# Performance work log

Measured on AMD Instinct MI355X. Metric: run time of the kernel, lower is better.

Reference implementation:

```python
import math
import jax, jax.numpy as jnp
from jax import lax
import numpy as np

B, C, M, N = 8, 512, 64, 64
DN = ('NCHW', 'OIHW', 'NCHW')


def dct_mat(n):
    # Orthonormal DCT-II basis, matching the torch construction.
    i = jnp.arange(n, dtype=jnp.float32)
    A = jnp.cos(jnp.outer(i, i + 0.5) * (math.pi / n)) * np.float32(math.sqrt(2.0 / n))
    return A.at[0].divide(np.float32(math.sqrt(2.0)))


def setup_inputs() -> dict:
    key = jax.random.key(0)
    ks = jax.random.split(key, 7)
    s = 0.05
    x = jax.random.normal(ks[0], (B, C, M, N), dtype=jnp.float32)
    # 4 conv branches, each: 1x1 512->128, 3x3 dil=2 128->128, 1x1 128->128
    W1 = jax.random.normal(ks[1], (4, 128, 512, 1, 1), dtype=jnp.float32) * s
    b1 = jax.random.normal(ks[2], (4, 128), dtype=jnp.float32) * s
    W2 = jax.random.normal(ks[3], (4, 128, 128, 3, 3), dtype=jnp.float32) * s
    b2 = jax.random.normal(ks[4], (4, 128), dtype=jnp.float32) * s
    W3 = jax.random.normal(ks[5], (4, 128, 128, 1, 1), dtype=jnp.float32) * s
    b3 = jax.random.normal(ks[6], (4, 128), dtype=jnp.float32) * s
    return {"x": x, "W1": W1, "b1": b1, "W2": W2, "b2": b2, "W3": W3, "b3": b3}


def dct3d_topk(x):
    b, c, m, n = x.shape
    Ac, Ar, Ak = dct_mat(n), dct_mat(m), dct_mat(c)
    # separable 3D DCT: along N, then M, then C
    t = jnp.einsum('kn,bcmn->bcmk', Ac, x)
    t = jnp.einsum('km,bcmn->bckn', Ar, t)
    D = jnp.einsum('kc,bcmn->bkmn', Ak, t)
    total = b * c * m * n
    absD = jnp.abs(D)
    s = jnp.sort(absD.reshape(-1))  # ascending; kth-largest = s[total-k]
    recons = []
    for k in (total // 4, total // 16, total // 64, total // 256):
        thr = s[total - k]
        Dm = jnp.where(absD >= thr, D, jnp.float32(0))
        y = jnp.einsum('kc,bkmn->bcmn', Ak, Dm)   # inverse along C
        y = jnp.einsum('km,bckn->bcmn', Ar, y)    # inverse along M
        y = jnp.einsum('kn,bcmk->bcmn', Ac, y)    # inverse along N
        recons.append(y)
    return jnp.stack(recons)  # [4, B, C, M, N]


def conv_branch(h, w1, c1, w2, c2, w3, c3):
    h = lax.conv_general_dilated(h, w1, (1, 1), 'VALID', dimension_numbers=DN)
    h = jax.nn.relu(h + c1[None, :, None, None])
    h = lax.conv_general_dilated(h, w2, (1, 1), ((2, 2), (2, 2)), rhs_dilation=(2, 2), dimension_numbers=DN)
    h = jax.nn.relu(h + c2[None, :, None, None])
    h = lax.conv_general_dilated(h, w3, (1, 1), 'VALID', dimension_numbers=DN)
    return jax.nn.relu(h + c3[None, :, None, None])


def reference(x, W1, b1, W2, b2, W3, b3):
    d = dct3d_topk(x)
    outs = [conv_branch(d[i], W1[i], b1[i], W2[i], b2[i], W3[i], b3[i]) for i in range(4)]
    w = jax.nn.softmax(jnp.concatenate(outs, axis=1), axis=1)
    return x * w + x
```

## Files before the change

### kernel.cpp

```cpp
#include <hip/hip_runtime.h>
#include <math.h>

#define NB   8
#define NC   512
#define SP   4096
#define TOT  16777216L
static const double PI_D = 3.14159265358979323846;

typedef short s16x8 __attribute__((ext_vector_type(8)));
typedef float f32x4 __attribute__((ext_vector_type(4)));
typedef unsigned short u16;

#define OFF_T    0L
#define OFF_CAND 0L
#define OFF_CNT  8388608L
#define OFF_P2   8392704L
#define OFF_P3   9441280L
#define OFF_H2R  9965568L
#define OFF_H3R  9969664L
#define OFF_H1P  0L
#define OFF_X2   8388608L
#define OFF_THI  16777216L
#define OFF_H1   16777216L
#define OFF_D    25165824L
#define OFF_H2   25165824L
#define OFF_AK   41943040L
#define OFF_AKH  42205184L
#define OFF_AKL  42336256L
#define OFF_ACT  42467328L
#define OFF_GBF  42468352L
#define OFF_W2A  42599424L
#define OFF_W3B  42894336L
#define OFF_HIST 42927104L
#define OFF_SEL  42937344L
#define OFF_THR  42937360L
#define OFF_AC   42937368L

__device__ inline u16 bfr(float x) {
    unsigned u = __float_as_uint(x);
    unsigned r = u + 0x7fffu + ((u >> 16) & 1u);
    return (u16)(r >> 16);
}
__device__ inline float bff(u16 h) { return __uint_as_float(((unsigned)h) << 16); }

#define MFMA(a, b, c) __builtin_amdgcn_mfma_f32_16x16x32_bf16((a), (b), (c), 0, 0, 0)

__global__ void k_ctab(float* __restrict__ ctab) {
    int m = blockIdx.x * 256 + threadIdx.x;
    if (m < 2048) ctab[m] = (float)cos(PI_D * (double)m / 1024.0);
}

__global__ void k_build_mats(const float* __restrict__ ctab,
                             u16* __restrict__ Akh, u16* __restrict__ Akl,
                             u16* __restrict__ AcT, float* __restrict__ Ac) {
    int idx = blockIdx.x * 256 + threadIdx.x;
    if (idx < 512 * 512) {
        int i = idx >> 9, j = idx & 511;
        float c = ctab[(i * (2 * j + 1)) & 2047];
        float f = c * (i == 0 ? 0.04419417382415922f : 0.0625f);
        u16 h = bfr(f);
        Akh[idx] = h;
        Akl[idx] = bfr(f - bff(h));
    }
    if (idx < 64 * 64) {
        int i = idx >> 6, j = idx & 63;
        float c = ctab[(8 * i * (2 * j + 1)) & 2047];
        Ac[idx] = c * (i == 0 ? 0.125f : 0.17677669529663687f);
        int n = idx >> 6, np = idx & 63;
        float w = ctab[(8 * np * (2 * n + 1)) & 2047];
        AcT[idx] = bfr(w * (np == 0 ? 0.125f : 0.17677669529663687f));
    }
}

__global__ void k_zero(unsigned* __restrict__ p, int n) {
    int i = blockIdx.x * 256 + threadIdx.x;
    if (i < n) p[i] = 0u;
}

__global__ __launch_bounds__(256, 2) void k_gmm(const float* __restrict__ W1,
                                                const u16* __restrict__ Akh, const u16* __restrict__ Akl,
                                                u16* __restrict__ G) {
    __shared__ __align__(16) short Wh[128 * 40];
    __shared__ __align__(16) short Wl[128 * 40];
    __shared__ __align__(16) short Qh[128 * 40];
    __shared__ __align__(16) short Ql[128 * 40];
    const int p0 = blockIdx.y * 128, kc0 = blockIdx.x * 128;
    const int tid = threadIdx.x;
    const int lane = tid & 63, wave = tid >> 6;
    const int fr = lane & 15, qd = lane >> 4;
    const int mq = (wave >> 1) * 64, nq = (wave & 1) * 64;
    f32x4 acc[4][4];
#pragma unroll
    for (int i = 0; i < 4; ++i)
#pragma unroll
        for (int j = 0; j < 4; ++j) acc[i][j] = (f32x4){0.f, 0.f, 0.f, 0.f};
    const float* Pg = W1 + (long)p0 * 512;
    const u16* Qgh = Akh + (long)kc0 * 512;
    const u16* Qgl = Akl + (long)kc0 * 512;
    const int r0 = tid >> 2, q40 = (tid & 3) * 8;
    float4 pa4[2], pb4[2];
    s16x8 qsh[2], qsl[2];
#pragma unroll
    for (int j = 0; j < 2; ++j) {
        int r = r0 + j * 64;
        const float* src = &Pg[(long)r * 512 + q40];
        pa4[j] = *(const float4*)src;
        pb4[j] = *(const float4*)(src + 4);
        qsh[j] = *(const s16x8*)&Qgh[(long)r * 512 + q40];
        qsl[j] = *(const s16x8*)&Qgl[(long)r * 512 + q40];
    }
    for (int ch = 0; ch < 16; ++ch) {
        __syncthreads();
#pragma unroll
        for (int j = 0; j < 2; ++j) {
            int r = r0 + j * 64;
            float f[8] = {pa4[j].x, pa4[j].y, pa4[j].z, pa4[j].w,
                          pb4[j].x, pb4[j].y, pb4[j].z, pb4[j].w};
            s16x8 vh, vl;
#pragma unroll
            for (int q = 0; q < 8; ++q) {
                u16 h = bfr(f[q]);
                vh[q] = (short)h;
                vl[q] = (short)bfr(f[q] - bff(h));
            }
            *(s16x8*)&Wh[r * 40 + q40] = vh;
            *(s16x8*)&Wl[r * 40 + q40] = vl;
            *(s16x8*)&Qh[r * 40 + q40] = qsh[j];
            *(s16x8*)&Ql[r * 40 + q40] = qsl[j];
        }
        __syncthreads();
        if (ch < 15) {
            const int kn = (ch + 1) * 32;
#pragma unroll
            for (int j = 0; j < 2; ++j) {
                int r = r0 + j * 64;
                const float* src = &Pg[(long)r * 512 + kn + q40];
                pa4[j] = *(const float4*)src;
                pb4[j] = *(const float4*)(src + 4);
                qsh[j] = *(const s16x8*)&Qgh[(long)r * 512 + kn + q40];
                qsl[j] = *(const s16x8*)&Qgl[(long)r * 512 + kn + q40];
            }
        }
        s16x8 qfh[4], qfl[4];
#pragma unroll
        for (int j = 0; j < 4; ++j) {
            qfh[j] = *(const s16x8*)&Qh[(nq + 16 * j + fr) * 40 + qd * 8];
            qfl[j] = *(const s16x8*)&Ql[(nq + 16 * j + fr) * 40 + qd * 8];
        }
#pragma unroll
        for (int i = 0; i < 4; ++i) {
            s16x8 wh = *(const s16x8*)&Wh[(mq + 16 * i + fr) * 40 + qd * 8];
            s16x8 wl = *(const s16x8*)&Wl[(mq + 16 * i + fr) * 40 + qd * 8];
#pragma unroll
            for (int j = 0; j < 4; ++j) {
                acc[i][j] = MFMA(wh, qfh[j], acc[i][j]);
                acc[i][j] = MFMA(wh, qfl[j], acc[i][j]);
                acc[i][j] = MFMA(wl, qfh[j], acc[i][j]);
            }
        }
    }
#pragma unroll
    for (int i = 0; i < 4; ++i)
#pragma unroll
        for (int j = 0; j < 4; ++j) {
            int rowb = mq + 16 * i + qd * 4;
            int col = kc0 + nq + 16 * j + fr;
#pragma unroll
            for (int r = 0; r < 4; ++r)
                G[(long)(p0 + rowb + r) * 512 + col] = bfr(acc[i][j][r]);
        }
}

__global__ void k_wprep(const float* __restrict__ W2, const float* __restrict__ W3,
                        u16* __restrict__ W2a, u16* __restrict__ W3b) {
    int idx = blockIdx.x * 256 + threadIdx.x;
    if (idx < 4 * 128 * 1152) {
        int k = idx % 1152;
        int oi = idx / 1152;
        int t = k >> 7, ci = k & 127;
        W2a[idx] = bfr(W2[((long)oi * 128 + ci) * 9 + t]);
    }
    if (idx < 65536) W3b[idx] = bfr(W3[idx]);
}

__global__ __launch_bounds__(256, 3) void k_tile_fwd(const float* __restrict__ in,
                                                     u16* __restrict__ out16,
                                                     const float* __restrict__ A64) {
    __shared__ __align__(16) float Ms[64][68];
    __shared__ __align__(16) float Ts[64][68];
    __shared__ __align__(16) float Ss[64][68];
    const int tid = threadIdx.x;
    const long tile = blockIdx.x;
    const float* __restrict__ src = in + tile * 4096;
    u16* __restrict__ dst = out16 + tile * 4096;
    for (int idx = tid; idx < 4096; idx += 256) {
        int r = idx >> 6, c = idx & 63;
        Ms[c][r] = A64[idx];
        Ts[r][c] = src[idx];
    }
    __syncthreads();
    const int tx = tid & 15, ty = tid >> 4;
    float acc[4][4];
#pragma unroll
    for (int i = 0; i < 4; ++i)
#pragma unroll
        for (int j = 0; j < 4; ++j) acc[i][j] = 0.f;
#pragma unroll 4
    for (int j = 0; j < 64; ++j) {
        float4 bv = *(const float4*)&Ms[j][tx * 4];
        float a0 = Ts[ty * 4 + 0][j], a1 = Ts[ty * 4 + 1][j];
        float a2 = Ts[ty * 4 + 2][j], a3 = Ts[ty * 4 + 3][j];
        acc[0][0] += a0 * bv.x; acc[0][1] += a0 * bv.y; acc[0][2] += a0 * bv.z; acc[0][3] += a0 * bv.w;
        acc[1][0] += a1 * bv.x; acc[1][1] += a1 * bv.y; acc[1][2] += a1 * bv.z; acc[1][3] += a1 * bv.w;
        acc[2][0] += a2 * bv.x; acc[2][1] += a2 * bv.y; acc[2][2] += a2 * bv.z; acc[2][3] += a2 * bv.w;
        acc[3][0] += a3 * bv.x; acc[3][1] += a3 * bv.y; acc[3][2] += a3 * bv.z; acc[3][3] += a3 * bv.w;
    }
#pragma unroll
    for (int i = 0; i < 4; ++i)
        *(float4*)&Ss[ty * 4 + i][tx * 4] = make_float4(acc[i][0], acc[i][1], acc[i][2], acc[i][3]);
    __syncthreads();
#pragma unroll
    for (int i = 0; i < 4; ++i)
#pragma unroll
        for (int j = 0; j < 4; ++j) acc[i][j] = 0.f;
#pragma unroll 4
    for (int j = 0; j < 64; ++j) {
        float4 av = *(const float4*)&Ms[j][ty * 4];
        float4 sv = *(const float4*)&Ss[j][tx * 4];
        acc[0][0] += av.x * sv.x; acc[0][1] += av.x * sv.y; acc[0][2] += av.x * sv.z; acc[0][3] += av.x * sv.w;
        acc[1][0] += av.y * sv.x; acc[1][1] += av.y * sv.y; acc[1][2] += av.y * sv.z; acc[1][3] += av.y * sv.w;
        acc[2][0] += av.z * sv.x; acc[2][1] += av.z * sv.y; acc[2][2] += av.z * sv.z; acc[2][3] += av.z * sv.w;
        acc[3][0] += av.w * sv.x; acc[3][1] += av.w * sv.y; acc[3][2] += av.w * sv.z; acc[3][3] += av.w * sv.w;
    }
#pragma unroll
    for (int i = 0; i < 4; ++i) {
        ushort4 pk;
        pk.x = bfr(acc[i][0]); pk.y = bfr(acc[i][1]);
        pk.z = bfr(acc[i][2]); pk.w = bfr(acc[i][3]);
        *(ushort4*)&dst[(ty * 4 + i) * 64 + tx * 4] = pk;
    }
}

__global__ __launch_bounds__(256) void k_tsplit(const u16* __restrict__ t16,
                                                u16* __restrict__ thi) {
    __shared__ float Ls[64][65];
    const int b = blockIdx.z, cg = blockIdx.y, pg = blockIdx.x;
    const int tid = threadIdx.x;
    const u16* src = t16 + ((long)b * 512 + cg * 64) * 4096 + pg * 64;
#pragma unroll
    for (int j = 0; j < 2; ++j) {
        int idx = tid + j * 256;
        int c = idx >> 3, p8 = (idx & 7) * 8;
        s16x8 v = *(const s16x8*)&src[(long)c * 4096 + p8];
#pragma unroll
        for (int q = 0; q < 8; ++q) Ls[c][p8 + q] = bff((u16)v[q]);
    }
    __syncthreads();
#pragma unroll
    for (int j = 0; j < 2; ++j) {
        int idx = tid + j * 256;
        int p = idx >> 3, c8 = idx & 7;
        s16x8 vh;
#pragma unroll
        for (int q = 0; q < 8; ++q) vh[q] = (short)bfr(Ls[c8 * 8 + q][p]);
        long addr = ((long)b * 4096 + pg * 64 + p) * 512 + cg * 64 + c8 * 8;
        *(s16x8*)&thi[addr] = vh;
    }
}

__global__ __launch_bounds__(256, 4) void k_cgemm(const u16* __restrict__ thi,
                                                  const u16* __restrict__ Akh, const u16* __restrict__ Akl,
                                                  float* __restrict__ D, unsigned* __restrict__ g1) {
    __shared__ __align__(16) short Ph[128 * 40];
    __shared__ __align__(16) short Qh[128 * 40];
    __shared__ __align__(16) short Ql[128 * 40];
    __shared__ unsigned hh[2048];
    const int b = blockIdx.z;
    const int p0 = blockIdx.y * 128, kc0 = blockIdx.x * 128;
    const int tid = threadIdx.x;
    const int lane = tid & 63, wave = tid >> 6;
    const int fr = lane & 15, qd = lane >> 4;
    const int mq = (wave >> 1) * 64, nq = (wave & 1) * 64;
    for (int t = tid; t < 2048; t += 256) hh[t] = 0u;
    f32x4 acc[4][4];
#pragma unroll
    for (int i = 0; i < 4; ++i)
#pragma unroll
        for (int j = 0; j < 4; ++j) acc[i][j] = (f32x4){0.f, 0.f, 0.f, 0.f};
    const u16* Pgh = thi + ((long)b * 4096 + p0) * 512;
    const u16* Qgh = Akh + (long)kc0 * 512;
    const u16* Qgl = Akl + (long)kc0 * 512;
    const int r0 = tid >> 2, q40 = (tid & 3) * 8;
    s16x8 psh[2], qsh[2], qsl[2];
#pragma unroll
    for (int j = 0; j < 2; ++j) {
        int r = r0 + j * 64;
        psh[j] = *(const s16x8*)&Pgh[(long)r * 512 + q40];
        qsh[j] = *(const s16x8*)&Qgh[(long)r * 512 + q40];
        qsl[j] = *(const s16x8*)&Qgl[(long)r * 512 + q40];
    }
    for (int ch = 0; ch < 16; ++ch) {
        __syncthreads();
#pragma unroll
        for (int j = 0; j < 2; ++j) {
            int r = r0 + j * 64;
            *(s16x8*)&Ph[r * 40 + q40] = psh[j];
            *(s16x8*)&Qh[r * 40 + q40] = qsh[j];
            *(s16x8*)&Ql[r * 40 + q40] = qsl[j];
        }
        __syncthreads();
        if (ch < 15) {
            const int kn = (ch + 1) * 32;
#pragma unroll
            for (int j = 0; j < 2; ++j) {
                int r = r0 + j * 64;
                psh[j] = *(const s16x8*)&Pgh[(long)r * 512 + kn + q40];
                qsh[j] = *(const s16x8*)&Qgh[(long)r * 512 + kn + q40];
                qsl[j] = *(const s16x8*)&Qgl[(long)r * 512 + kn + q40];
            }
        }
        s16x8 qfh[4], qfl[4];
#pragma unroll
        for (int j = 0; j < 4; ++j) {
            qfh[j] = *(const s16x8*)&Qh[(nq + 16 * j + fr) * 40 + qd * 8];
            qfl[j] = *(const s16x8*)&Ql[(nq + 16 * j + fr) * 40 + qd * 8];
        }
#pragma unroll
        for (int i = 0; i < 4; ++i) {
            s16x8 ph = *(const s16x8*)&Ph[(mq + 16 * i + fr) * 40 + qd * 8];
#pragma unroll
            for (int j = 0; j < 4; ++j) {
                acc[i][j] = MFMA(ph, qfh[j], acc[i][j]);
                acc[i][j] = MFMA(ph, qfl[j], acc[i][j]);
            }
        }
    }
#pragma unroll
    for (int i = 0; i < 4; ++i)
#pragma unroll
        for (int j = 0; j < 4; ++j) {
            int rowb = mq + 16 * i + qd * 4;
            int col = kc0 + nq + 16 * j + fr;
#pragma unroll
            for (int r = 0; r < 4; ++r) {
                float v = acc[i][j][r];
                D[((long)b * 4096 + p0 + rowb + r) * 512 + col] = v;
                unsigned bin = __float_as_uint(fabsf(v)) >> 19;
                atomicAdd(&hh[bin & 2047u], 1u << ((bin >> 11) << 4));
            }
        }
    __syncthreads();
    for (int t = tid; t < 2048; t += 256) {
        unsigned c = hh[t];
        unsigned lo = c & 0xffffu, hi = c >> 16;
        if (lo) atomicAdd(&g1[t], lo);
        if (hi) atomicAdd(&g1[t + 2048], hi);
    }
}

__global__ void k_scan1(const unsigned* __restrict__ hist, unsigned* __restrict__ sel) {
    __shared__ unsigned chunk[256];
    __shared__ unsigned above[256];
    const int t = threadIdx.x;
    unsigned s = 0;
#pragma unroll
    for (int j = 0; j < 16; ++j) s += hist[t * 16 + j];
    chunk[t] = s;
    __syncthreads();
    if (t == 0) {
        unsigned a = 0;
        for (int c = 255; c >= 0; --c) { above[c] = a; a += chunk[c]; }
    }
    __syncthreads();
    const unsigned kv[4] = {4194304u, 1048576u, 262144u, 65536u};
    unsigned run = above[t];
    for (int j = 15; j >= 0; --j) {
        unsigned bin = t * 16 + j;
        unsigned hb = hist[bin];
        unsigned Sab = run;
        run += hb;
#pragma unroll
        for (int i = 0; i < 4; ++i)
            if (run >= kv[i] && Sab < kv[i]) { sel[i] = bin; sel[4 + i] = kv[i] - Sab; }
    }
}

__global__ __launch_bounds__(256) void k_compact(const float4* __restrict__ D,
                                                 const unsigned* __restrict__ sel,
                                                 unsigned* __restrict__ cand,
                                                 unsigned* __restrict__ cnt) {
    __shared__ unsigned lctr;
    if (threadIdx.x == 0) lctr = 0u;
    __syncthreads();
    const unsigned p0 = sel[0], p1 = sel[1], p2 = sel[2], p3 = sel[3];
    const int lane = threadIdx.x & 63;
    unsigned* slice = cand + (long)blockIdx.x * 4096;
    const long n4 = TOT / 4;
    for (long idx = (long)blockIdx.x * 256 + threadIdx.x; idx < n4; idx += (long)gridDim.x * 256) {
        float4 v = D[idx];
        float f[4] = {v.x, v.y, v.z, v.w};
#pragma unroll
        for (int q = 0; q < 4; ++q) {
            unsigned u = __float_as_uint(fabsf(f[q]));
            unsigned pre = u >> 19;
            bool m = (pre == p0) | (pre == p1) | (pre == p2) | (pre == p3);
            unsigned long long mask = __ballot(m);
            if (mask) {
                int leader = __ffsll((long long)mask) - 1;
                unsigned base = 0;
                if (lane == leader) base = atomicAdd(&lctr, (unsigned)__popcll(mask));
                base = (unsigned)__shfl((int)base, leader);
                if (m) {
                    unsigned pos = base + (unsigned)__popcll(mask & ((1ULL << lane) - 1ULL));
                    if (pos < 4096u) slice[pos] = u;
                }
            }
        }
    }
    __syncthreads();
    if (threadIdx.x == 0) cnt[blockIdx.x] = lctr < 4096u ? lctr : 4096u;
}

__global__ __launch_bounds__(256) void k_hist2c(const unsigned* __restrict__ cand,
                                                const unsigned* __restrict__ cnt,
                                                const unsigned* __restrict__ sel,
                                                unsigned* __restrict__ partial) {
    __shared__ unsigned h[4096];
    for (int i = threadIdx.x; i < 4096; i += 256) h[i] = 0u;
    __syncthreads();
    const unsigned p0 = sel[0], p1 = sel[1], p2 = sel[2], p3 = sel[3];
    for (int s = 0; s < 8; ++s) {
        int slice = blockIdx.x * 8 + s;
        unsigned n = cnt[slice];
        const unsigned* L = cand + (long)slice * 4096;
        for (unsigned i = threadIdx.x; i < n; i += 256) {
            unsigned u = L[i];
            unsigned pre = u >> 19, mid = (u >> 9) & 1023u;
            if (pre == p0) atomicAdd(&h[mid], 1u);
            else if (pre == p1) atomicAdd(&h[1024 + mid], 1u);
            else if (pre == p2) atomicAdd(&h[2048 + mid], 1u);
            else if (pre == p3) atomicAdd(&h[3072 + mid], 1u);
        }
    }
    __syncthreads();
    unsigned* dst = partial + (long)blockIdx.x * 4096;
    for (int i = threadIdx.x; i < 4096; i += 256) dst[i] = h[i];
}

__global__ __launch_bounds__(256) void k_red(const unsigned* __restrict__ partial,
                                             unsigned* __restrict__ out, int nbins, int nrows) {
    int bin = blockIdx.x * 256 + threadIdx.x;
    if (bin >= nbins) return;
    unsigned s = 0;
#pragma unroll 16
    for (int r = 0; r < nrows; ++r) s += partial[(long)r * nbins + bin];
    out[bin] = s;
}

__global__ void k_scan2(const unsigned* __restrict__ hist2, unsigned* __restrict__ sel) {
    __shared__ unsigned chunk[256];
    __shared__ unsigned above[256];
    const int t = threadIdx.x;
    for (int i = 0; i < 4; ++i) {
        const unsigned* h = hist2 + i * 1024;
        unsigned r = sel[4 + i];
        unsigned s = h[t * 4] + h[t * 4 + 1] + h[t * 4 + 2] + h[t * 4 + 3];
        chunk[t] = s;
        __syncthreads();
        if (t == 0) {
            unsigned a = 0;
            for (int c = 255; c >= 0; --c) { above[c] = a; a += chunk[c]; }
        }
        __syncthreads();
        unsigned run = above[t];
        for (int j = 3; j >= 0; --j) {
            unsigned bin = t * 4 + j;
            unsigned hb = h[bin];
            unsigned Sab = run;
            run += hb;
            if (run >= r && Sab < r) { sel[8 + i] = bin; sel[12 + i] = r - Sab; }
        }
        __syncthreads();
    }
}

__global__ __launch_bounds__(256) void k_hist3c(const unsigned* __restrict__ cand,
                                                const unsigned* __restrict__ cnt,
                                                const unsigned* __restrict__ sel,
                                                unsigned* __restrict__ partial) {
    __shared__ unsigned h[2048];
    for (int i = threadIdx.x; i < 2048; i += 256) h[i] = 0u;
    __syncthreads();
    unsigned pre2[4];
#pragma unroll
    for (int i = 0; i < 4; ++i) pre2[i] = (sel[i] << 10) | sel[8 + i];
    for (int s = 0; s < 8; ++s) {
        int slice = blockIdx.x * 8 + s;
        unsigned n = cnt[slice];
        const unsigned* L = cand + (long)slice * 4096;
        for (unsigned i = threadIdx.x; i < n; i += 256) {
            unsigned u = L[i];
            unsigned p = u >> 9, low = u & 511u;
            if (p == pre2[0]) atomicAdd(&h[low], 1u);
            else if (p == pre2[1]) atomicAdd(&h[512 + low], 1u);
            else if (p == pre2[2]) atomicAdd(&h[1024 + low], 1u);
            else if (p == pre2[3]) atomicAdd(&h[1536 + low], 1u);
        }
    }
    __syncthreads();
    unsigned* dst = partial + (long)blockIdx.x * 2048;
    for (int i = threadIdx.x; i < 2048; i += 256) dst[i] = h[i];
}

__global__ void k_scan3(const unsigned* __restrict__ hist3, const unsigned* __restrict__ sel,
                        float* __restrict__ thr) {
    __shared__ unsigned chunk[256];
    __shared__ unsigned above[256];
    const int t = threadIdx.x;
    for (int i = 0; i < 4; ++i) {
        const unsigned* h = hist3 + i * 512;
        unsigned r = sel[12 + i];
        unsigned s = h[t * 2] + h[t * 2 + 1];
        chunk[t] = s;
        __syncthreads();
        if (t == 0) {
            unsigned a = 0;
            for (int c = 255; c >= 0; --c) { above[c] = a; a += chunk[c]; }
        }
        __syncthreads();
        unsigned run = above[t];
        for (int j = 1; j >= 0; --j) {
            unsigned bin = t * 2 + j;
            unsigned hb = h[bin];
            unsigned Sab = run;
            run += hb;
            if (run >= r && Sab < r)
                thr[i] = __uint_as_float((sel[i] << 19) | (sel[8 + i] << 9) | bin);
        }
        __syncthreads();
    }
}

__global__ __launch_bounds__(256, 4) void k_conv1(const float* __restrict__ D, const u16* __restrict__ Gb,
                                                  const float* __restrict__ thrp, u16* __restrict__ h1pre) {
    __shared__ __align__(16) short Pt[128 * 40];
    __shared__ __align__(16) short Qt[128 * 40];
    const int b = blockIdx.z, br = blockIdx.y, p0 = blockIdx.x * 128;
    const int z2 = br * 8 + b;
    const float thr = thrp[br];
    const int tid = threadIdx.x;
    const int lane = tid & 63, wave = tid >> 6;
    const int fr = lane & 15, qd = lane >> 4;
    const int mq = (wave >> 1) * 64, nq = (wave & 1) * 64;
    f32x4 acc[4][4];
#pragma unroll
    for (int i = 0; i < 4; ++i)
#pragma unroll
        for (int j = 0; j < 4; ++j) acc[i][j] = (f32x4){0.f, 0.f, 0.f, 0.f};
    const float* Pg = D + ((long)b * 4096 + p0) * 512;
    const u16* Qg = Gb + (long)br * 65536;
    const int r0 = tid >> 2, q40 = (tid & 3) * 8;
    float4 da[2], db[2];
#pragma unroll
    for (int j = 0; j < 2; ++j) {
        const float* src = &Pg[(long)(r0 + j * 64) * 512 + q40];
        da[j] = *(const float4*)src;
        db[j] = *(const float4*)(src + 4);
    }
    for (int ch = 0; ch < 16; ++ch) {
        const int k0 = ch * 32;
        __syncthreads();
#pragma unroll
        for (int j = 0; j < 2; ++j) {
            int r = r0 + j * 64;
            s16x8 m;
            float f[8] = {da[j].x, da[j].y, da[j].z, da[j].w, db[j].x, db[j].y, db[j].z, db[j].w};
#pragma unroll
            for (int q = 0; q < 8; ++q) m[q] = (short)(fabsf(f[q]) >= thr ? bfr(f[q]) : (u16)0);
            *(s16x8*)&Pt[r * 40 + q40] = m;
            *(s16x8*)&Qt[r * 40 + q40] = *(const s16x8*)&Qg[(long)r * 512 + k0 + q40];
        }
        __syncthreads();
        if (ch < 15) {
            const int kn = k0 + 32;
#pragma unroll
            for (int j = 0; j < 2; ++j) {
                const float* src = &Pg[(long)(r0 + j * 64) * 512 + kn + q40];
                da[j] = *(const float4*)src;
                db[j] = *(const float4*)(src + 4);
            }
        }
        s16x8 qb[4];
#pragma unroll
        for (int j = 0; j < 4; ++j) qb[j] = *(const s16x8*)&Qt[(nq + 16 * j + fr) * 40 + qd * 8];
#pragma unroll
        for (int i = 0; i < 4; ++i) {
            s16x8 pa = *(const s16x8*)&Pt[(mq + 16 * i + fr) * 40 + qd * 8];
#pragma unroll
            for (int j = 0; j < 4; ++j) acc[i][j] = MFMA(pa, qb[j], acc[i][j]);
        }
    }
#pragma unroll
    for (int i = 0; i < 4; ++i)
#pragma unroll
        for (int j = 0; j < 4; ++j) {
            int rowb = p0 + mq + 16 * i + qd * 4;
            int o = nq + 16 * j + fr;
            ushort4 pk;
            pk.x = bfr(acc[i][j][0]); pk.y = bfr(acc[i][j][1]);
            pk.z = bfr(acc[i][j][2]); pk.w = bfr(acc[i][j][3]);
            *(ushort4*)&h1pre[((long)z2 * 128 + o) * 4096 + rowb] = pk;
        }
}

__global__ __launch_bounds__(256, 4) void k_idct1(const u16* __restrict__ h1pre, const u16* __restrict__ AcT,
                                                  u16* __restrict__ X2) {
    __shared__ __align__(16) short Pt[128 * 72];
    __shared__ __align__(16) short Qt[64 * 72];
    const int b = blockIdx.z, br = blockIdx.y, m0 = blockIdx.x * 128;
    const int z2 = br * 8 + b;
    const int tid = threadIdx.x;
    const int lane = tid & 63, wave = tid >> 6;
    const int fr = lane & 15, qd = lane >> 4;
    const int mq = wave * 32;
    const u16* Pg = h1pre + (long)z2 * 524288 + (long)m0 * 64;
    f32x4 acc[2][4];
#pragma unroll
    for (int i = 0; i < 2; ++i)
#pragma unroll
        for (int j = 0; j < 4; ++j) acc[i][j] = (f32x4){0.f, 0.f, 0.f, 0.f};
#pragma unroll
    for (int j = 0; j < 4; ++j) {
        int idx = tid + j * 256;
        int r = idx >> 3, q8 = (idx & 7) * 8;
        *(s16x8*)&Pt[r * 72 + q8] = *(const s16x8*)&Pg[(long)r * 64 + q8];
    }
#pragma unroll
    for (int j = 0; j < 2; ++j) {
        int idx = tid + j * 256;
        int r = idx >> 3, q8 = (idx & 7) * 8;
        *(s16x8*)&Qt[r * 72 + q8] = *(const s16x8*)&AcT[(long)r * 64 + q8];
    }
    __syncthreads();
#pragma unroll
    for (int ks = 0; ks < 2; ++ks) {
        s16x8 pa[2], qb[4];
#pragma unroll
        for (int i = 0; i < 2; ++i) pa[i] = *(const s16x8*)&Pt[(mq + 16 * i + fr) * 72 + ks * 32 + qd * 8];
#pragma unroll
        for (int j = 0; j < 4; ++j) qb[j] = *(const s16x8*)&Qt[(16 * j + fr) * 72 + ks * 32 + qd * 8];
#pragma unroll
        for (int i = 0; i < 2; ++i)
#pragma unroll
            for (int j = 0; j < 4; ++j) acc[i][j] = MFMA(pa[i], qb[j], acc[i][j]);
    }
#pragma unroll
    for (int i = 0; i < 2; ++i)
#pragma unroll
        for (int j = 0; j < 4; ++j) {
            int Rb = m0 + mq + 16 * i + qd * 4;
            int o = Rb >> 6, y = Rb & 63;
            int xo = 16 * j + fr;
            ushort4 pk;
            pk.x = bfr(acc[i][j][0]); pk.y = bfr(acc[i][j][1]);
            pk.z = bfr(acc[i][j][2]); pk.w = bfr(acc[i][j][3]);
            *(ushort4*)&X2[(long)z2 * 524288 + ((long)xo * 128 + o) * 64 + y] = pk;
        }
}

__global__ __launch_bounds__(256, 4) void k_idct2(const u16* __restrict__ X2, const u16* __restrict__ AcT,
                                                  const float* __restrict__ b1, u16* __restrict__ h1) {
    __shared__ __align__(16) short Pt[128 * 72];
    __shared__ __align__(16) short Qt[64 * 72];
    const int b = blockIdx.z, br = blockIdx.y, m0 = blockIdx.x * 128;
    const int z2 = br * 8 + b;
    const int tid = threadIdx.x;
    const int lane = tid & 63, wave = tid >> 6;
    const int fr = lane & 15, qd = lane >> 4;
    const int mq = wave * 32;
    const u16* Pg = X2 + (long)z2 * 524288 + (long)m0 * 64;
    f32x4 acc[2][4];
#pragma unroll
    for (int i = 0; i < 2; ++i)
#pragma unroll
        for (int j = 0; j < 4; ++j) acc[i][j] = (f32x4){0.f, 0.f, 0.f, 0.f};
#pragma unroll
    for (int j = 0; j < 4; ++j) {
        int idx = tid + j * 256;
        int r = idx >> 3, q8 = (idx & 7) * 8;
        *(s16x8*)&Pt[r * 72 + q8] = *(const s16x8*)&Pg[(long)r * 64 + q8];
    }
#pragma unroll
    for (int j = 0; j < 2; ++j) {
        int idx = tid + j * 256;
        int r = idx >> 3, q8 = (idx & 7) * 8;
        *(s16x8*)&Qt[r * 72 + q8] = *(const s16x8*)&AcT[(long)r * 64 + q8];
    }
    __syncthreads();
#pragma unroll
    for (int ks = 0; ks < 2; ++ks) {
        s16x8 pa[2], qb[4];
#pragma unroll
        for (int i = 0; i < 2; ++i) pa[i] = *(const s16x8*)&Pt[(mq + 16 * i + fr) * 72 + ks * 32 + qd * 8];
#pragma unroll
        for (int j = 0; j < 4; ++j) qb[j] = *(const s16x8*)&Qt[(16 * j + fr) * 72 + ks * 32 + qd * 8];
#pragma unroll
        for (int i = 0; i < 2; ++i)
#pragma unroll
            for (int j = 0; j < 4; ++j) acc[i][j] = MFMA(pa[i], qb[j], acc[i][j]);
    }
#pragma unroll
    for (int i = 0; i < 2; ++i)
#pragma unroll
        for (int j = 0; j < 4; ++j) {
            int Rb = m0 + mq + 16 * i + qd * 4;
            int xo = Rb >> 7, o = Rb & 127;
            int yo = 16 * j + fr;
            ushort4 pk;
            const float* bg = b1 + br * 128 + o;
            pk.x = bfr(fmaxf(acc[i][j][0] + bg[0], 0.f));
            pk.y = bfr(fmaxf(acc[i][j][1] + bg[1], 0.f));
            pk.z = bfr(fmaxf(acc[i][j][2] + bg[2], 0.f));
            pk.w = bfr(fmaxf(acc[i][j][3] + bg[3], 0.f));
            *(ushort4*)&h1[(long)z2 * 524288 + ((long)yo * 64 + xo) * 128 + o] = pk;
        }
}

__global__ __launch_bounds__(256, 4) void k_conv2(const u16* __restrict__ h1, const u16* __restrict__ W2a,
                                                  const float* __restrict__ b2, u16* __restrict__ h2) {
    __shared__ __align__(16) short Pt[128 * 40];
    __shared__ __align__(16) short Qt[128 * 40];
    const int b = blockIdx.z, br = blockIdx.y, y0 = blockIdx.x * 2;
    const int z2 = br * 8 + b;
    const int tid = threadIdx.x;
    const int lane = tid & 63, wave = tid >> 6;
    const int fr = lane & 15, qd = lane >> 4;
    const int mq = (wave >> 1) * 64, nq = (wave & 1) * 64;
    f32x4 acc[4][4];
#pragma unroll
    for (int i = 0; i < 4; ++i)
#pragma unroll
        for (int j = 0; j < 4; ++j) acc[i][j] = (f32x4){0.f, 0.f, 0.f, 0.f};
    const u16* hb = h1 + (long)z2 * 524288;
    const u16* Qg = W2a + (long)br * 147456;
    const int r0 = tid >> 2, q40 = (tid & 3) * 8;
    s16x8 preg[2];
    auto loadP = [&](int ch) {
        const int t9 = ch >> 2, ci0 = (ch & 3) * 32;
        const int ky = t9 / 3, kx = t9 - 3 * ky;
        const int dy = 2 * ky - 2, dx = 2 * kx - 2;
#pragma unroll
        for (int j = 0; j < 2; ++j) {
            int r = r0 + j * 64;
            int ry = r >> 6, xx = r & 63;
            int ysrc = y0 + ry + dy, xsrc = xx + dx;
            s16x8 v = {0, 0, 0, 0, 0, 0, 0, 0};
            if ((unsigned)ysrc < 64u && (unsigned)xsrc < 64u)
                v = *(const s16x8*)&hb[((long)ysrc * 64 + xsrc) * 128 + ci0 + q40];
            preg[j] = v;
        }
    };
    loadP(0);
    for (int ch = 0; ch < 36; ++ch) {
        __syncthreads();
#pragma unroll
        for (int j = 0; j < 2; ++j) {
            int r = r0 + j * 64;
            *(s16x8*)&Pt[r * 40 + q40] = preg[j];
            *(s16x8*)&Qt[r * 40 + q40] = *(const s16x8*)&Qg[(long)r * 1152 + ch * 32 + q40];
        }
        __syncthreads();
        if (ch < 35) loadP(ch + 1);
        s16x8 qb[4];
#pragma unroll
        for (int j = 0; j < 4; ++j) qb[j] = *(const s16x8*)&Qt[(nq + 16 * j + fr) * 40 + qd * 8];
#pragma unroll
        for (int i = 0; i < 4; ++i) {
            s16x8 pa = *(const s16x8*)&Pt[(mq + 16 * i + fr) * 40 + qd * 8];
#pragma unroll
            for (int j = 0; j < 4; ++j) acc[i][j] = MFMA(pa, qb[j], acc[i][j]);
        }
    }
#pragma unroll
    for (int i = 0; i < 4; ++i)
#pragma unroll
        for (int j = 0; j < 4; ++j) {
            int rowb = mq + 16 * i + qd * 4;
            int o = nq + 16 * j + fr;
            float bb = b2[br * 128 + o];
#pragma unroll
            for (int r = 0; r < 4; ++r) {
                float v = fmaxf(acc[i][j][r] + bb, 0.f);
                h2[(long)z2 * 524288 + ((long)y0 * 64 + rowb + r) * 128 + o] = bfr(v);
            }
        }
}

__global__ __launch_bounds__(256, 4) void k_conv3(const u16* __restrict__ h2, const u16* __restrict__ W3b,
                                                  const float* __restrict__ b3, u16* __restrict__ lgn) {
    __shared__ __align__(16) short buf[18432];
    short* Pt = buf;
    short* Qt = buf + 5120;
    const int b = blockIdx.z, br = blockIdx.y, p0 = blockIdx.x * 128;
    const int z2 = br * 8 + b;
    const int m0 = blockIdx.x * 2;
    const int tid = threadIdx.x;
    const int lane = tid & 63, wave = tid >> 6;
    const int fr = lane & 15, qd = lane >> 4;
    const int mq = (wave >> 1) * 64, nq = (wave & 1) * 64;
    f32x4 acc[4][4];
#pragma unroll
    for (int i = 0; i < 4; ++i)
#pragma unroll
        for (int j = 0; j < 4; ++j) acc[i][j] = (f32x4){0.f, 0.f, 0.f, 0.f};
    const u16* Pg = h2 + (long)z2 * 524288 + (long)p0 * 128;
    const u16* Qg = W3b + (long)br * 16384;
    for (int ch = 0; ch < 4; ++ch) {
        const int k0 = ch * 32;
        __syncthreads();
#pragma unroll
        for (int j = 0; j < 2; ++j) {
            int idx = tid + j * 256;
            int r = idx >> 2, q4 = (idx & 3) * 8;
            *(s16x8*)&Pt[r * 40 + q4] = *(const s16x8*)&Pg[(long)r * 128 + k0 + q4];
            *(s16x8*)&Qt[r * 40 + q4] = *(const s16x8*)&Qg[(long)r * 128 + k0 + q4];
        }
        __syncthreads();
        s16x8 pa[4], qb[4];
#pragma unroll
        for (int i = 0; i < 4; ++i) {
            pa[i] = *(const s16x8*)&Pt[(mq + 16 * i + fr) * 40 + qd * 8];
            qb[i] = *(const s16x8*)&Qt[(nq + 16 * i + fr) * 40 + qd * 8];
        }
#pragma unroll
        for (int i = 0; i < 4; ++i)
#pragma unroll
            for (int j = 0; j < 4; ++j) acc[i][j] = MFMA(pa[i], qb[j], acc[i][j]);
    }
    __syncthreads();
#pragma unroll
    for (int i = 0; i < 4; ++i)
#pragma unroll
        for (int j = 0; j < 4; ++j) {
            int l = mq + 16 * i + qd * 4;
            int mrow = l >> 6, nn = l & 63;
            int o = nq + 16 * j + fr;
            float bb = b3[br * 128 + o];
            ushort4 pk;
            pk.x = bfr(fmaxf(acc[i][j][0] + bb, 0.f));
            pk.y = bfr(fmaxf(acc[i][j][1] + bb, 0.f));
            pk.z = bfr(fmaxf(acc[i][j][2] + bb, 0.f));
            pk.w = bfr(fmaxf(acc[i][j][3] + bb, 0.f));
            *(ushort4*)&buf[mrow * 9216 + o * 72 + nn] = pk;
        }
    __syncthreads();
#pragma unroll
    for (int t = 0; t < 16; ++t) {
        int u = tid + t * 256;
        int mrow = u >> 11;
        int rem = u & 2047;
        int cl = rem >> 4, n4 = (rem & 15) << 2;
        ushort4 v = *(const ushort4*)&buf[mrow * 9216 + cl * 72 + n4];
        long dst = (((long)b * 64 + m0 + mrow) * 512 + br * 128 + cl) * 64 + n4;
        *(ushort4*)&lgn[dst] = v;
    }
}

__global__ __launch_bounds__(256) void k_final(const float* __restrict__ x, const u16* __restrict__ lgn,
                                               float* __restrict__ out) {
    const int b = blockIdx.y, m = blockIdx.x;
    const int tid = threadIdx.x;
    const int csub = tid >> 3, oct = tid & 7;
    const u16* L = lgn + ((long)b * 64 + m) * 512 * 64;
    __shared__ float redm[32][64];
    __shared__ float reds[32][64];
    __shared__ float Mf[64], Sf[64];
    float mx[8], sm[8];
#pragma unroll
    for (int q = 0; q < 8; ++q) { mx[q] = -1e30f; sm[q] = 0.f; }
#pragma unroll 4
    for (int k = 0; k < 16; ++k) {
        int c = csub * 16 + k;
        s16x8 v8 = *(const s16x8*)&L[c * 64 + oct * 8];
#pragma unroll
        for (int q = 0; q < 8; ++q) {
            float v = bff((u16)v8[q]);
            float mn = fmaxf(mx[q], v);
            sm[q] = sm[q] * __expf(mx[q] - mn) + __expf(v - mn);
            mx[q] = mn;
        }
    }
#pragma unroll
    for (int q = 0; q < 8; ++q) {
        redm[csub][oct * 8 + q] = mx[q];
        reds[csub][oct * 8 + q] = sm[q];
    }
    __syncthreads();
    if (tid < 64) {
        float M = -1e30f;
#pragma unroll 8
        for (int g = 0; g < 32; ++g) M = fmaxf(M, redm[g][tid]);
        float S = 0.f;
#pragma unroll 8
        for (int g = 0; g < 32; ++g) S += reds[g][tid] * __expf(redm[g][tid] - M);
        Mf[tid] = M;
        Sf[tid] = 1.0f / S;
    }
    __syncthreads();
    float Mv[8], Iv[8];
#pragma unroll
    for (int q = 0; q < 8; ++q) { Mv[q] = Mf[oct * 8 + q]; Iv[q] = Sf[oct * 8 + q]; }
    const long xb = (long)b * 512 * 4096 + m * 64 + oct * 8;
#pragma unroll 4
    for (int k = 0; k < 16; ++k) {
        int c = csub * 16 + k;
        s16x8 v8 = *(const s16x8*)&L[c * 64 + oct * 8];
        long a = xb + (long)c * 4096;
        float4 x0 = *(const float4*)&x[a];
        float4 x1 = *(const float4*)&x[a + 4];
        float xf[8] = {x0.x, x0.y, x0.z, x0.w, x1.x, x1.y, x1.z, x1.w};
        float r[8];
#pragma unroll
        for (int q = 0; q < 8; ++q) {
            float w = __expf(bff((u16)v8[q]) - Mv[q]) * Iv[q];
            r[q] = xf[q] * w + xf[q];
        }
        *(float4*)&out[a] = make_float4(r[0], r[1], r[2], r[3]);
        *(float4*)&out[a + 4] = make_float4(r[4], r[5], r[6], r[7]);
    }
}

extern "C" void kernel_launch(void* const* d_in, const int* in_sizes, int n_in,
                              void* d_out, int out_size, void* d_ws, size_t ws_size,
                              hipStream_t stream) {
    (void)in_sizes; (void)n_in; (void)out_size; (void)ws_size;
    const float* x  = (const float*)d_in[0];
    const float* W1 = (const float*)d_in[1];
    const float* b1 = (const float*)d_in[2];
    const float* W2 = (const float*)d_in[3];
    const float* b2 = (const float*)d_in[4];
    const float* W3 = (const float*)d_in[5];
    const float* b3 = (const float*)d_in[6];
    float* out = (float*)d_out;
    float* ws = (float*)d_ws;

    u16*   t16  = (u16*)(ws + OFF_T);
    unsigned* cand = (unsigned*)(ws + OFF_CAND);
    unsigned* cnt  = (unsigned*)(ws + OFF_CNT);
    unsigned* p2   = (unsigned*)(ws + OFF_P2);
    unsigned* p3   = (unsigned*)(ws + OFF_P3);
    unsigned* h2r  = (unsigned*)(ws + OFF_H2R);
    unsigned* h3r  = (unsigned*)(ws + OFF_H3R);
    u16*   h1pre= (u16*)(ws + OFF_H1P);
    u16*   lgn  = (u16*)(ws + OFF_H1P);
    u16*   X2   = (u16*)(ws + OFF_X2);
    u16*   thi  = (u16*)(ws + OFF_THI);
    u16*   h1   = (u16*)(ws + OFF_H1);
    float* D    = ws + OFF_D;
    float* ctab = ws + OFF_D;
    u16*   h2   = (u16*)(ws + OFF_H2);
    u16*   Akh  = (u16*)(ws + OFF_AKH);
    u16*   Akl  = (u16*)(ws + OFF_AKL);
    u16*   AcT  = (u16*)(ws + OFF_ACT);
    u16*   Gb   = (u16*)(ws + OFF_GBF);
    u16*   W2a  = (u16*)(ws + OFF_W2A);
    u16*   W3b  = (u16*)(ws + OFF_W3B);
    unsigned* hist1 = (unsigned*)(ws + OFF_HIST);
    unsigned* sel   = (unsigned*)(ws + OFF_SEL);
    float* thr      = ws + OFF_THR;
    float* Ac       = ws + OFF_AC;

    k_ctab<<<8, 256, 0, stream>>>(ctab);
    k_build_mats<<<1024, 256, 0, stream>>>(ctab, Akh, Akl, AcT, Ac);
    k_zero<<<16, 256, 0, stream>>>(hist1, 4096);
    k_gmm<<<dim3(4, 4), 256, 0, stream>>>(W1, Akh, Akl, Gb);
    k_wprep<<<2304, 256, 0, stream>>>(W2, W3, W2a, W3b);

    k_tile_fwd<<<4096, 256, 0, stream>>>(x, t16, Ac);
    k_tsplit<<<dim3(64, 8, 8), 256, 0, stream>>>(t16, thi);
    k_cgemm<<<dim3(4, 32, 8), 256, 0, stream>>>(thi, Akh, Akl, D, hist1);

    k_scan1<<<1, 256, 0, stream>>>(hist1, sel);
    k_compact<<<2048, 256, 0, stream>>>((const float4*)D, sel, cand, cnt);
    k_hist2c<<<256, 256, 0, stream>>>(cand, cnt, sel, p2);
    k_red<<<16, 256, 0, stream>>>(p2, h2r, 4096, 256);
    k_scan2<<<1, 256, 0, stream>>>(h2r, sel);
    k_hist3c<<<256, 256, 0, stream>>>(cand, cnt, sel, p3);
    k_red<<<8, 256, 0, stream>>>(p3, h3r, 2048, 256);
    k_scan3<<<1, 256, 0, stream>>>(h3r, sel, thr);

    k_conv1<<<dim3(32, 4, 8), 256, 0, stream>>>(D, Gb, thr, h1pre);
    k_idct1<<<dim3(64, 4, 8), 256, 0, stream>>>(h1pre, AcT, X2);
    k_idct2<<<dim3(64, 4, 8), 256, 0, stream>>>(X2, AcT, b1, h1);
    k_conv2<<<dim3(32, 4, 8), 256, 0, stream>>>(h1, W2a, b2, h2);
    k_conv3<<<dim3(32, 4, 8), 256, 0, stream>>>(h2, W3b, b3, lgn);

    k_final<<<dim3(64, 8), 256, 0, stream>>>(x, lgn, out);
}
```

Baseline: 506.0 us.

## Move per-tile 2D forward DCT from FP32 FMA to split-bf16 MFMA

```diff
diff --git a/kernel.cpp b/kernel.cpp
--- a/kernel.cpp
+++ b/kernel.cpp
@@ -34,7 +34,8 @@
 #define OFF_HIST 42927104L
 #define OFF_SEL  42937344L
 #define OFF_THR  42937360L
-#define OFF_AC   42937368L
+#define OFF_ACH  42937368L
+#define OFF_ACL  42939416L
 
 __device__ inline u16 bfr(float x) {
     unsigned u = __float_as_uint(x);
@@ -52,7 +53,7 @@
 
 __global__ void k_build_mats(const float* __restrict__ ctab,
                              u16* __restrict__ Akh, u16* __restrict__ Akl,
-                             u16* __restrict__ AcT, float* __restrict__ Ac) {
+                             u16* __restrict__ AcT, u16* __restrict__ Ach, u16* __restrict__ Acl) {
     int idx = blockIdx.x * 256 + threadIdx.x;
     if (idx < 512 * 512) {
         int i = idx >> 9, j = idx & 511;
@@ -65,7 +66,10 @@
     if (idx < 64 * 64) {
         int i = idx >> 6, j = idx & 63;
         float c = ctab[(8 * i * (2 * j + 1)) & 2047];
-        Ac[idx] = c * (i == 0 ? 0.125f : 0.17677669529663687f);
+        float a = c * (i == 0 ? 0.125f : 0.17677669529663687f);
+        u16 ah = bfr(a);
+        Ach[idx] = ah;
+        Acl[idx] = bfr(a - bff(ah));
         int n = idx >> 6, np = idx & 63;
         float w = ctab[(8 * np * (2 * n + 1)) & 2047];
         AcT[idx] = bfr(w * (np == 0 ? 0.125f : 0.17677669529663687f));
@@ -185,60 +189,118 @@
 
 __global__ __launch_bounds__(256, 3) void k_tile_fwd(const float* __restrict__ in,
                                                      u16* __restrict__ out16,
-                                                     const float* __restrict__ A64) {
-    __shared__ __align__(16) float Ms[64][68];
-    __shared__ __align__(16) float Ts[64][68];
-    __shared__ __align__(16) float Ss[64][68];
+                                                     const u16* __restrict__ Ach,
+                                                     const u16* __restrict__ Acl) {
+    __shared__ __align__(16) short Xb[64 * 72];
+    __shared__ __align__(16) short Ah[64 * 72];
+    __shared__ __align__(16) short Al[64 * 72];
+    __shared__ __align__(16) short Uh[64 * 72];
+    __shared__ __align__(16) short Ul[64 * 72];
     const int tid = threadIdx.x;
     const long tile = blockIdx.x;
     const float* __restrict__ src = in + tile * 4096;
     u16* __restrict__ dst = out16 + tile * 4096;
-    for (int idx = tid; idx < 4096; idx += 256) {
-        int r = idx >> 6, c = idx & 63;
-        Ms[c][r] = A64[idx];
-        Ts[r][c] = src[idx];
-    }
-    __syncthreads();
-    const int tx = tid & 15, ty = tid >> 4;
-    float acc[4][4];
-#pragma unroll
-    for (int i = 0; i < 4; ++i)
-#pragma unroll
-        for (int j = 0; j < 4; ++j) acc[i][j] = 0.f;
-#pragma unroll 4
-    for (int j = 0; j < 64; ++j) {
-        float4 bv = *(const float4*)&Ms[j][tx * 4];
-        float a0 = Ts[ty * 4 + 0][j], a1 = Ts[ty * 4 + 1][j];
-        float a2 = Ts[ty * 4 + 2][j], a3 = Ts[ty * 4 + 3][j];
-        acc[0][0] += a0 * bv.x; acc[0][1] += a0 * bv.y; acc[0][2] += a0 * bv.z; acc[0][3] += a0 * bv.w;
-        acc[1][0] += a1 * bv.x; acc[1][1] += a1 * bv.y; acc[1][2] += a1 * bv.z; acc[1][3] += a1 * bv.w;
-        acc[2][0] += a2 * bv.x; acc[2][1] += a2 * bv.y; acc[2][2] += a2 * bv.z; acc[2][3] += a2 * bv.w;
-        acc[3][0] += a3 * bv.x; acc[3][1] += a3 * bv.y; acc[3][2] += a3 * bv.z; acc[3][3] += a3 * bv.w;
-    }
-#pragma unroll
-    for (int i = 0; i < 4; ++i)
-        *(float4*)&Ss[ty * 4 + i][tx * 4] = make_float4(acc[i][0], acc[i][1], acc[i][2], acc[i][3]);
-    __syncthreads();
-#pragma unroll
-    for (int i = 0; i < 4; ++i)
-#pragma unroll
-        for (int j = 0; j < 4; ++j) acc[i][j] = 0.f;
-#pragma unroll 4
-    for (int j = 0; j < 64; ++j) {
-        float4 av = *(const float4*)&Ms[j][ty * 4];
-        float4 sv = *(const float4*)&Ss[j][tx * 4];
-        acc[0][0] += av.x * sv.x; acc[0][1] += av.x * sv.y; acc[0][2] += av.x * sv.z; acc[0][3] += av.x * sv.w;
-        acc[1][0] += av.y * sv.x; acc[1][1] += av.y * sv.y; acc[1][2] += av.y * sv.z; acc[1][3] += av.y * sv.w;
-        acc[2][0] += av.z * sv.x; acc[2][1] += av.z * sv.y; acc[2][2] += av.z * sv.z; acc[2][3] += av.z * sv.w;
-        acc[3][0] += av.w * sv.x; acc[3][1] += av.w * sv.y; acc[3][2] += av.w * sv.z; acc[3][3] += av.w * sv.w;
-    }
-#pragma unroll
-    for (int i = 0; i < 4; ++i) {
-        ushort4 pk;
-        pk.x = bfr(acc[i][0]); pk.y = bfr(acc[i][1]);
-        pk.z = bfr(acc[i][2]); pk.w = bfr(acc[i][3]);
-        *(ushort4*)&dst[(ty * 4 + i) * 64 + tx * 4] = pk;
-    }
+    {
+        const int r = tid >> 2, q16 = (tid & 3) * 16;
+        const float* s = &src[r * 64 + q16];
+        float4 f0 = *(const float4*)s;
+        float4 f1 = *(const float4*)(s + 4);
+        float4 f2 = *(const float4*)(s + 8);
+        float4 f3 = *(const float4*)(s + 12);
+        s16x8 v0, v1;
+        v0[0] = (short)bfr(f0.x); v0[1] = (short)bfr(f0.y);
+        v0[2] = (short)bfr(f0.z); v0[3] = (short)bfr(f0.w);
+        v0[4] = (short)bfr(f1.x); v0[5] = (short)bfr(f1.y);
+        v0[6] = (short)bfr(f1.z); v0[7] = (short)bfr(f1.w);
+        v1[0] = (short)bfr(f2.x); v1[1] = (short)bfr(f2.y);
+        v1[2] = (short)bfr(f2.z); v1[3] = (short)bfr(f2.w);
+        v1[4] = (short)bfr(f3.x); v1[5] = (short)bfr(f3.y);
+        v1[6] = (short)bfr(f3.z); v1[7] = (short)bfr(f3.w);
+        *(s16x8*)&Xb[r * 72 + q16] = v0;
+        *(s16x8*)&Xb[r * 72 + q16 + 8] = v1;
+        *(s16x8*)&Ah[r * 72 + q16] = *(const s16x8*)&Ach[r * 64 + q16];
+        *(s16x8*)&Ah[r * 72 + q16 + 8] = *(const s16x8*)&Ach[r * 64 + q16 + 8];
+        *(s16x8*)&Al[r * 72 + q16] = *(const s16x8*)&Acl[r * 64 + q16];
+        *(s16x8*)&Al[r * 72 + q16 + 8] = *(const s16x8*)&Acl[r * 64 + q16 + 8];
+    }
+    __syncthreads();
+    const int lane = tid & 63, wave = tid >> 6;
+    const int fr = lane & 15, qd = lane >> 4;
+    const int mq = (wave >> 1) * 32, nq = (wave & 1) * 32;
+    f32x4 a1[2][2];
+#pragma unroll
+    for (int i = 0; i < 2; ++i)
+#pragma unroll
+        for (int j = 0; j < 2; ++j) a1[i][j] = (f32x4){0.f, 0.f, 0.f, 0.f};
+#pragma unroll
+    for (int ks = 0; ks < 2; ++ks) {
+        const int k0 = ks * 32 + qd * 8;
+        s16x8 xp[2];
+#pragma unroll
+        for (int i = 0; i < 2; ++i) xp[i] = *(const s16x8*)&Xb[(mq + 16 * i + fr) * 72 + k0];
+#pragma unroll
+        for (int j = 0; j < 2; ++j) {
+            s16x8 qh = *(const s16x8*)&Ah[(nq + 16 * j + fr) * 72 + k0];
+            s16x8 ql = *(const s16x8*)&Al[(nq + 16 * j + fr) * 72 + k0];
+#pragma unroll
+            for (int i = 0; i < 2; ++i) {
+                a1[i][j] = MFMA(xp[i], qh, a1[i][j]);
+                a1[i][j] = MFMA(xp[i], ql, a1[i][j]);
+            }
+        }
+    }
+#pragma unroll
+    for (int i = 0; i < 2; ++i)
+#pragma unroll
+        for (int j = 0; j < 2; ++j) {
+            int k1 = nq + 16 * j + fr;
+            int mb = mq + 16 * i + qd * 4;
+            ushort4 ph, pl;
+            float v0 = a1[i][j][0], v1 = a1[i][j][1], v2 = a1[i][j][2], v3 = a1[i][j][3];
+            ph.x = bfr(v0); ph.y = bfr(v1); ph.z = bfr(v2); ph.w = bfr(v3);
+            pl.x = bfr(v0 - bff(ph.x)); pl.y = bfr(v1 - bff(ph.y));
+            pl.z = bfr(v2 - bff(ph.z)); pl.w = bfr(v3 - bff(ph.w));
+            *(ushort4*)&Uh[k1 * 72 + mb] = ph;
+            *(ushort4*)&Ul[k1 * 72 + mb] = pl;
+        }
+    __syncthreads();
+    f32x4 a2[2][2];
+#pragma unroll
+    for (int i = 0; i < 2; ++i)
+#pragma unroll
+        for (int j = 0; j < 2; ++j) a2[i][j] = (f32x4){0.f, 0.f, 0.f, 0.f};
+#pragma unroll
+    for (int ks = 0; ks < 2; ++ks) {
+        const int k0 = ks * 32 + qd * 8;
+        s16x8 uh[2], ul[2];
+#pragma unroll
+        for (int i = 0; i < 2; ++i) {
+            uh[i] = *(const s16x8*)&Uh[(mq + 16 * i + fr) * 72 + k0];
+            ul[i] = *(const s16x8*)&Ul[(mq + 16 * i + fr) * 72 + k0];
+        }
+#pragma unroll
+        for (int j = 0; j < 2; ++j) {
+            s16x8 qh = *(const s16x8*)&Ah[(nq + 16 * j + fr) * 72 + k0];
+            s16x8 ql = *(const s16x8*)&Al[(nq + 16 * j + fr) * 72 + k0];
+#pragma unroll
+            for (int i = 0; i < 2; ++i) {
+                a2[i][j] = MFMA(uh[i], qh, a2[i][j]);
+                a2[i][j] = MFMA(uh[i], ql, a2[i][j]);
+                a2[i][j] = MFMA(ul[i], qh, a2[i][j]);
+            }
+        }
+    }
+#pragma unroll
+    for (int i = 0; i < 2; ++i)
+#pragma unroll
+        for (int j = 0; j < 2; ++j) {
+            int k2 = nq + 16 * j + fr;
+            int nb = mq + 16 * i + qd * 4;
+            ushort4 pk;
+            pk.x = bfr(a2[i][j][0]); pk.y = bfr(a2[i][j][1]);
+            pk.z = bfr(a2[i][j][2]); pk.w = bfr(a2[i][j][3]);
+            *(ushort4*)&dst[k2 * 64 + nb] = pk;
+        }
 }
 
 __global__ __launch_bounds__(256) void k_tsplit(const u16* __restrict__ t16,
@@ -968,15 +1030,16 @@
     unsigned* hist1 = (unsigned*)(ws + OFF_HIST);
     unsigned* sel   = (unsigned*)(ws + OFF_SEL);
     float* thr      = ws + OFF_THR;
-    float* Ac       = ws + OFF_AC;
+    u16*   Ach  = (u16*)(ws + OFF_ACH);
+    u16*   Acl  = (u16*)(ws + OFF_ACL);
 
     k_ctab<<<8, 256, 0, stream>>>(ctab);
-    k_build_mats<<<1024, 256, 0, stream>>>(ctab, Akh, Akl, AcT, Ac);
+    k_build_mats<<<1024, 256, 0, stream>>>(ctab, Akh, Akl, AcT, Ach, Acl);
     k_zero<<<16, 256, 0, stream>>>(hist1, 4096);
     k_gmm<<<dim3(4, 4), 256, 0, stream>>>(W1, Akh, Akl, Gb);
     k_wprep<<<2304, 256, 0, stream>>>(W2, W3, W2a, W3b);
 
-    k_tile_fwd<<<4096, 256, 0, stream>>>(x, t16, Ac);
+    k_tile_fwd<<<4096, 256, 0, stream>>>(x, t16, Ach, Acl);
     k_tsplit<<<dim3(64, 8, 8), 256, 0, stream>>>(t16, thi);
     k_cgemm<<<dim3(4, 32, 8), 256, 0, stream>>>(thi, Akh, Akl, D, hist1);
 
```

Result: faster. 478.3 us (-5.5%).
